# Performance work log

Measured on AMD Instinct MI355X. Metric: run time of the kernel, lower is better.

The kernel has to match this reference:

```python
import jax, jax.numpy as jnp
import numpy as np

B, N, D_IN, H = 4, 4096, 3072, 64
ADJ_DENSITY = 0.01


def _layernorm(x, g, b, eps=1e-5):
    mu = jnp.mean(x, axis=-1, keepdims=True)
    var = jnp.var(x, axis=-1, keepdims=True)
    return (x - mu) * jax.lax.rsqrt(var + eps) * g + b


def _gat(x, W, adj, concat):
    # x: [B, N, H], W: [H, H], adj: [N, N]
    Wh = jnp.matmul(x, W)                                   # [B, N, H]
    scores = jnp.einsum('bnh,bmh->bnm', Wh, Wh) / np.sqrt(H)  # [B, N, N]
    scores = jnp.where(adj > 0, scores, jnp.float32(-1e9))
    attn = jax.nn.softmax(scores, axis=2)                   # dropout: eval no-op
    h_prime = jnp.matmul(attn, Wh)                          # [B, N, H]
    return jax.nn.elu(h_prime) if concat else h_prime


def setup_inputs() -> dict:
    key = jax.random.key(0)
    ks = jax.random.split(key, 18)
    adj = (jax.random.uniform(ks[0], (N, N)) < ADJ_DENSITY).astype(jnp.float32)
    adj = jnp.maximum(adj, jnp.eye(N, dtype=jnp.float32))   # self loops

    def xavier(k, shape, gain=1.0):
        bound = gain * np.sqrt(6.0 / (shape[0] + shape[1]))
        return jax.random.uniform(k, shape, jnp.float32, -bound, bound)

    return {
        'stim_features': jax.random.normal(ks[1], (B, D_IN), jnp.float32),
        'adj': adj,
        'W_enc1': xavier(ks[2], (D_IN, 2 * H)),
        'b_enc1': jnp.zeros((2 * H,), jnp.float32),
        'ln_g': jnp.ones((2 * H,), jnp.float32),
        'ln_b': jnp.zeros((2 * H,), jnp.float32),
        'W_enc2': xavier(ks[3], (2 * H, H)),
        'b_enc2': jnp.zeros((H,), jnp.float32),
        'voxel_emb': jax.random.normal(ks[4], (N, H), jnp.float32) * 0.01,
        'W_gat1': xavier(ks[5], (H, H), gain=1.414),
        'W_gat2': xavier(ks[6], (H, H), gain=1.414),
        'skip1_W': xavier(ks[7], (H, H)),
        'skip1_b': jnp.zeros((H,), jnp.float32),
        'skip2_W': xavier(ks[8], (H, H)),
        'skip2_b': jnp.zeros((H,), jnp.float32),
        'ro_W': xavier(ks[9], (H, 1)),
        'ro_b': jnp.zeros((1,), jnp.float32),
    }


def reference(stim_features, adj, W_enc1, b_enc1, ln_g, ln_b, W_enc2, b_enc2,
              voxel_emb, W_gat1, W_gat2, skip1_W, skip1_b, skip2_W, skip2_b,
              ro_W, ro_b):
    # stim encoder: Linear -> LayerNorm -> GELU -> (Dropout eval) -> Linear
    g = stim_features @ W_enc1 + b_enc1                     # [B, 2H]
    g = _layernorm(g, ln_g, ln_b)
    g = jax.nn.gelu(g, approximate=False)
    g = g @ W_enc2 + b_enc2                                 # [B, H]

    x = g[:, None, :] + voxel_emb[None, :, :]               # [B, N, H]

    x_res = x
    x = _gat(x, W_gat1, adj, concat=True)
    x = x + (x_res @ skip1_W + skip1_b)

    x_res = x
    x = _gat(x, W_gat2, adj, concat=False)
    x = x + (x_res @ skip2_W + skip2_b)

    pred = (x @ ro_W + ro_b)[..., 0]                        # [B, N]
    return pred
```

## Files before the change

kernel.cpp:

```cpp
#include <hip/hip_runtime.h>
#include <math.h>

#define NB 4
#define NV 4096
#define DIN 3072
#define HD 64
#define CAP 80

typedef unsigned short u16;
typedef unsigned int u32;
typedef _Float16 h2 __attribute__((ext_vector_type(2)));

__device__ __forceinline__ float fdot2u(u32 v, u32 q, float c) {
#if __has_builtin(__builtin_amdgcn_fdot2)
  return __builtin_amdgcn_fdot2(__builtin_bit_cast(h2, v), __builtin_bit_cast(h2, q), c, false);
#else
  h2 a = __builtin_bit_cast(h2, v), b = __builtin_bit_cast(h2, q);
  return c + (float)a[0] * (float)b[0] + (float)a[1] * (float)b[1];
#endif
}

__device__ __forceinline__ h2 shx(h2 v, int off) {
  return __builtin_bit_cast(h2, (u32)__shfl_xor((int)__builtin_bit_cast(u32, v), off, 64));
}

__global__ __launch_bounds__(256) void pre_kernel(
    const float* __restrict__ adj, int* __restrict__ cnt, int* __restrict__ cols,
    const float* __restrict__ stim, const float* __restrict__ W1, float* __restrict__ part) {
  int bid = blockIdx.x;
  int t = threadIdx.x;
  if (bid < NV) {
    int row = bid;
    int l = t & 63, w = t >> 6;
    __shared__ int wtot[4];
    __shared__ int stot;
    const float4* p = (const float4*)(adj + (size_t)row * NV);
    float4 v0 = p[t], v1 = p[t + 256], v2 = p[t + 512], v3 = p[t + 768];
    int c = (v0.x > 0.f) + (v0.y > 0.f) + (v0.z > 0.f) + (v0.w > 0.f) +
            (v1.x > 0.f) + (v1.y > 0.f) + (v1.z > 0.f) + (v1.w > 0.f) +
            (v2.x > 0.f) + (v2.y > 0.f) + (v2.z > 0.f) + (v2.w > 0.f) +
            (v3.x > 0.f) + (v3.y > 0.f) + (v3.z > 0.f) + (v3.w > 0.f);
    int val = c;
#pragma unroll
    for (int off = 1; off < 64; off <<= 1) {
      int tmp = __shfl_up(val, off, 64);
      if (l >= off) val += tmp;
    }
    if (l == 63) wtot[w] = val;
    __syncthreads();
    int base = 0;
    for (int i = 0; i < w; ++i) base += wtot[i];
    if (t == 255) {
      int s = base + val;
      s = s > CAP ? CAP : s;
      cnt[row] = s;
      stot = s;
    }
    int o = base + (val - c);
    int* cr = cols + row * CAP;
#define EMIT(vv, jj) if ((vv) > 0.f) { if (o < CAP) cr[o] = (jj); ++o; }
    int j0 = t * 4, j1 = (t + 256) * 4, j2 = (t + 512) * 4, j3 = (t + 768) * 4;
    EMIT(v0.x, j0) EMIT(v0.y, j0 + 1) EMIT(v0.z, j0 + 2) EMIT(v0.w, j0 + 3)
    EMIT(v1.x, j1) EMIT(v1.y, j1 + 1) EMIT(v1.z, j1 + 2) EMIT(v1.w, j1 + 3)
    EMIT(v2.x, j2) EMIT(v2.y, j2 + 1) EMIT(v2.z, j2 + 2) EMIT(v2.w, j2 + 3)
    EMIT(v3.x, j3) EMIT(v3.y, j3 + 1) EMIT(v3.z, j3 + 2) EMIT(v3.w, j3 + 3)
#undef EMIT
    __syncthreads();
    if (t < CAP && t >= stot) cr[t] = 0;
  } else {
    int e = bid - NV;
    int c = e % 24;
    int b = e / 24;
    int j = t & 127, h = t >> 7;
    int k0 = c * 128 + h * 64;
    float acc = 0.f;
#pragma unroll 8
    for (int k = 0; k < 64; ++k)
      acc += stim[b * DIN + k0 + k] * W1[(size_t)(k0 + k) * 128 + j];
    part[((b * 24 + c) * 2 + h) * 128 + j] = acc;
  }
}

__global__ __launch_bounds__(128) void enc_b_kernel(
    const float* __restrict__ part, const float* __restrict__ b1,
    const float* __restrict__ lng, const float* __restrict__ lnb,
    const float* __restrict__ W2, const float* __restrict__ b2, float* __restrict__ g) {
  int b = blockIdx.x;
  int t = threadIdx.x;
  float hv = 0.f;
  for (int c = 0; c < 48; ++c) hv += part[(b * 48 + c) * 128 + t];
  hv += b1[t];
  __shared__ float act[128];
  __shared__ float red[128];
  __shared__ float s_mu, s_var;
  act[t] = hv;
  red[t] = hv;
  __syncthreads();
  for (int s = 64; s > 0; s >>= 1) {
    if (t < s) red[t] += red[t + s];
    __syncthreads();
  }
  if (t == 0) s_mu = red[0] * (1.f / 128.f);
  __syncthreads();
  float dv = act[t] - s_mu;
  red[t] = dv * dv;
  __syncthreads();
  for (int s = 64; s > 0; s >>= 1) {
    if (t < s) red[t] += red[t + s];
    __syncthreads();
  }
  if (t == 0) s_var = red[0] * (1.f / 128.f);
  __syncthreads();
  float y = (act[t] - s_mu) * rsqrtf(s_var + 1e-5f) * lng[t] + lnb[t];
  act[t] = 0.5f * y * (1.f + erff(y * 0.70710678118f));
  __syncthreads();
  if (t < 64) {
    float a2 = 0.f;
    for (int k = 0; k < 128; ++k) a2 += act[k] * W2[k * 64 + t];
    g[b * 64 + t] = a2 + b2[t];
  }
}

template <int LAYER>
__global__ __launch_bounds__(256) void whsk_kernel(
    const float* __restrict__ g, const float* __restrict__ emb, const float* __restrict__ xin,
    const float* __restrict__ Wg, const float* __restrict__ Sw, const float* __restrict__ Sb,
    u16* __restrict__ Whh, float* __restrict__ Sk) {
  __shared__ float wgt[4096];
  __shared__ float swt[4096];
  __shared__ float xst[64 * 33];
  __shared__ float sbs[64];
  int tid = threadIdx.x;
  for (int i = tid; i < 1024; i += 256) {
    ((float4*)wgt)[i] = ((const float4*)Wg)[i];
    ((float4*)swt)[i] = ((const float4*)Sw)[i];
  }
  if (tid < 64) sbs[tid] = Sb[tid];
  int base = blockIdx.x * 32;
  int b = base >> 12;
  for (int i4 = tid; i4 < 512; i4 += 256) {
    int rr = i4 >> 4, k0 = (i4 & 15) * 4;
    int grow = base + rr;
    float4 v;
    if (LAYER == 1) {
      int n = grow & (NV - 1);
      float4 gv = *(const float4*)(g + b * 64 + k0);
      float4 ev = *(const float4*)(emb + (size_t)n * 64 + k0);
      v = make_float4(gv.x + ev.x, gv.y + ev.y, gv.z + ev.z, gv.w + ev.w);
    } else {
      v = *(const float4*)(xin + (size_t)grow * 64 + k0);
    }
    xst[(k0 + 0) * 33 + rr] = v.x;
    xst[(k0 + 1) * 33 + rr] = v.y;
    xst[(k0 + 2) * 33 + rr] = v.z;
    xst[(k0 + 3) * 33 + rr] = v.w;
  }
  __syncthreads();
  int cg = tid & 15;
  int r0 = tid >> 4;
  float4 aw0 = make_float4(0, 0, 0, 0), as0 = make_float4(0, 0, 0, 0);
  float4 aw1 = make_float4(0, 0, 0, 0), as1 = make_float4(0, 0, 0, 0);
#pragma unroll 4
  for (int k = 0; k < 64; ++k) {
    float4 wv = *(const float4*)&wgt[k * 64 + 4 * cg];
    float4 sv = *(const float4*)&swt[k * 64 + 4 * cg];
    float x0 = xst[k * 33 + r0];
    float x1 = xst[k * 33 + r0 + 16];
    aw0.x = fmaf(x0, wv.x, aw0.x); aw0.y = fmaf(x0, wv.y, aw0.y);
    aw0.z = fmaf(x0, wv.z, aw0.z); aw0.w = fmaf(x0, wv.w, aw0.w);
    as0.x = fmaf(x0, sv.x, as0.x); as0.y = fmaf(x0, sv.y, as0.y);
    as0.z = fmaf(x0, sv.z, as0.z); as0.w = fmaf(x0, sv.w, as0.w);
    aw1.x = fmaf(x1, wv.x, aw1.x); aw1.y = fmaf(x1, wv.y, aw1.y);
    aw1.z = fmaf(x1, wv.z, aw1.z); aw1.w = fmaf(x1, wv.w, aw1.w);
    as1.x = fmaf(x1, sv.x, as1.x); as1.y = fmaf(x1, sv.y, as1.y);
    as1.z = fmaf(x1, sv.z, as1.z); as1.w = fmaf(x1, sv.w, as1.w);
  }
  float4 sb4 = *(const float4*)&sbs[4 * cg];
  int grow0 = base + r0, grow1 = base + r0 + 16;
  ushort4 h0, h1;
  h0.x = __builtin_bit_cast(u16, (_Float16)aw0.x);
  h0.y = __builtin_bit_cast(u16, (_Float16)aw0.y);
  h0.z = __builtin_bit_cast(u16, (_Float16)aw0.z);
  h0.w = __builtin_bit_cast(u16, (_Float16)aw0.w);
  h1.x = __builtin_bit_cast(u16, (_Float16)aw1.x);
  h1.y = __builtin_bit_cast(u16, (_Float16)aw1.y);
  h1.z = __builtin_bit_cast(u16, (_Float16)aw1.z);
  h1.w = __builtin_bit_cast(u16, (_Float16)aw1.w);
  *(ushort4*)(Whh + (size_t)grow0 * 64 + 4 * cg) = h0;
  *(ushort4*)(Whh + (size_t)grow1 * 64 + 4 * cg) = h1;
  *(float4*)(Sk + (size_t)grow0 * 64 + 4 * cg) =
      make_float4(as0.x + sb4.x, as0.y + sb4.y, as0.z + sb4.z, as0.w + sb4.w);
  *(float4*)(Sk + (size_t)grow1 * 64 + 4 * cg) =
      make_float4(as1.x + sb4.x, as1.y + sb4.y, as1.z + sb4.z, as1.w + sb4.w);
}

template <bool ELU1>
__global__ __launch_bounds__(256) void attn_kernel(
    const u16* __restrict__ Whh, const float* __restrict__ Sk,
    const int* __restrict__ cnt, const int* __restrict__ cols, float* __restrict__ xout,
    const float* __restrict__ roW, const float* __restrict__ rob, float* __restrict__ out) {
  int tid = threadIdx.x;
  int lane = tid & 63;
  int w = tid >> 6;
  int bid = blockIdx.x;
  int x = bid & 7;
  int gidx = bid >> 3;
  int b = x >> 1;
  int n = __builtin_amdgcn_readfirstlane((x & 1) * 2048 + gidx * 4 + w);
  int wid = b * NV + n;
  const u16* whhbase = Whh + (size_t)b * (NV * HD);
  int nn = __builtin_amdgcn_readfirstlane(cnt[n]);
  const int* cl = cols + n * CAP;
  int q = lane & 3;
  int gq = lane >> 2;

  const uint4* qr = (const uint4*)(whhbase + (size_t)n * HD);
  uint4 QA = qr[q];
  uint4 QB = qr[q + 4];

  float s[5], p[5];
  uint4 SA0, SB0, SA1, SB1, SA2, SB2;
#define SCORE_BLOCK(jb, SAv, SBv)                                                                \
  {                                                                                              \
    int j = (jb) * 16 + gq;                                                                      \
    int m = cl[j];                                                                               \
    const uint4* vr = (const uint4*)(whhbase + (size_t)m * HD);                                  \
    SAv = vr[q];                                                                                 \
    SBv = vr[q + 4];                                                                             \
    float t = 0.f;                                                                               \
    t = fdot2u(SAv.x, QA.x, t);                                                                  \
    t = fdot2u(SAv.y, QA.y, t);                                                                  \
    t = fdot2u(SAv.z, QA.z, t);                                                                  \
    t = fdot2u(SAv.w, QA.w, t);                                                                  \
    t = fdot2u(SBv.x, QB.x, t);                                                                  \
    t = fdot2u(SBv.y, QB.y, t);                                                                  \
    t = fdot2u(SBv.z, QB.z, t);                                                                  \
    t = fdot2u(SBv.w, QB.w, t);                                                                  \
    t += __shfl_xor(t, 1, 64);                                                                   \
    t += __shfl_xor(t, 2, 64);                                                                   \
    s[jb] = (j < nn) ? t * 0.125f : -1e30f;                                                      \
  }

  SCORE_BLOCK(0, SA0, SB0)
  SCORE_BLOCK(1, SA1, SB1)
  SCORE_BLOCK(2, SA2, SB2)
  s[3] = -1e30f;
  s[4] = -1e30f;
  bool tail = (nn > 48);
  if (tail) {
    uint4 TA, TB;
    SCORE_BLOCK(3, TA, TB)
    SCORE_BLOCK(4, TA, TB)
  }
#undef SCORE_BLOCK

  float mx = fmaxf(fmaxf(fmaxf(s[0], s[1]), fmaxf(s[2], s[3])), s[4]);
  mx = fmaxf(mx, __shfl_xor(mx, 4, 64));
  mx = fmaxf(mx, __shfl_xor(mx, 8, 64));
  mx = fmaxf(mx, __shfl_xor(mx, 16, 64));
  mx = fmaxf(mx, __shfl_xor(mx, 32, 64));
  float sum = 0.f;
#pragma unroll
  for (int jb = 0; jb < 5; ++jb) {
    p[jb] = (jb * 16 + gq < nn) ? __expf(s[jb] - mx) : 0.f;
    sum += p[jb];
  }
  sum += __shfl_xor(sum, 4, 64);
  sum += __shfl_xor(sum, 8, 64);
  sum += __shfl_xor(sum, 16, 64);
  sum += __shfl_xor(sum, 32, 64);
  float inv = 1.f / sum;

  h2 aa[8];
#pragma unroll
  for (int k = 0; k < 8; ++k) aa[k] = h2{(_Float16)0, (_Float16)0};
#define PV_ACC(pp, Av, Bv)                                                                       \
  {                                                                                              \
    _Float16 pf = (_Float16)(pp);                                                                \
    h2 ph = {pf, pf};                                                                            \
    aa[0] += __builtin_bit_cast(h2, (Av).x) * ph;                                                \
    aa[1] += __builtin_bit_cast(h2, (Av).y) * ph;                                                \
    aa[2] += __builtin_bit_cast(h2, (Av).z) * ph;                                                \
    aa[3] += __builtin_bit_cast(h2, (Av).w) * ph;                                                \
    aa[4] += __builtin_bit_cast(h2, (Bv).x) * ph;                                                \
    aa[5] += __builtin_bit_cast(h2, (Bv).y) * ph;                                                \
    aa[6] += __builtin_bit_cast(h2, (Bv).z) * ph;                                                \
    aa[7] += __builtin_bit_cast(h2, (Bv).w) * ph;                                                \
  }
  PV_ACC(p[0], SA0, SB0)
  PV_ACC(p[1], SA1, SB1)
  PV_ACC(p[2], SA2, SB2)
  if (tail) {
    int m3 = cl[48 + gq];
    const uint4* vr3 = (const uint4*)(whhbase + (size_t)m3 * HD);
    uint4 A3 = vr3[q], B3 = vr3[q + 4];
    PV_ACC(p[3], A3, B3)
    if (nn > 64) {
      int m4 = cl[64 + gq];
      const uint4* vr4 = (const uint4*)(whhbase + (size_t)m4 * HD);
      uint4 A4 = vr4[q], B4 = vr4[q + 4];
      PV_ACC(p[4], A4, B4)
    }
  }
#undef PV_ACC

  bool g1 = (gq & 1) != 0;
  h2 bb[4];
#pragma unroll
  for (int i = 0; i < 4; ++i) {
    h2 k = g1 ? aa[i + 4] : aa[i];
    h2 u = g1 ? aa[i] : aa[i + 4];
    bb[i] = k + shx(u, 4);
  }
  bool g2 = (gq & 2) != 0;
  h2 cc[2];
#pragma unroll
  for (int i = 0; i < 2; ++i) {
    h2 k = g2 ? bb[i + 2] : bb[i];
    h2 u = g2 ? bb[i] : bb[i + 2];
    cc[i] = k + shx(u, 8);
  }
  bool g4 = (gq & 4) != 0;
  h2 dd;
  {
    h2 k = g4 ? cc[1] : cc[0];
    h2 u = g4 ? cc[0] : cc[1];
    dd = k + shx(u, 16);
  }
  dd = dd + shx(dd, 32);
  int a = 8 * q + 32 * (gq & 1) + 4 * ((gq >> 1) & 1) + 2 * ((gq >> 2) & 1);
  float f0 = (float)dd[0] * inv;
  float f1 = (float)dd[1] * inv;

  size_t obase = (size_t)wid * HD;
  float2 sk2 = *(const float2*)(Sk + obase + a);
  if (ELU1) {
    float o0 = (f0 > 0.f ? f0 : (__expf(f0) - 1.f)) + sk2.x;
    float o1 = (f1 > 0.f ? f1 : (__expf(f1) - 1.f)) + sk2.y;
    if ((gq & 8) == 0) *(float2*)(xout + obase + a) = make_float2(o0, o1);
  } else {
    float2 ro2 = *(const float2*)(roW + a);
    float wsp = (f0 + sk2.x) * ro2.x + (f1 + sk2.y) * ro2.y;
    wsp += __shfl_xor(wsp, 1, 64);
    wsp += __shfl_xor(wsp, 2, 64);
    wsp += __shfl_xor(wsp, 4, 64);
    wsp += __shfl_xor(wsp, 8, 64);
    wsp += __shfl_xor(wsp, 16, 64);
    if (lane == 0) out[wid] = wsp + rob[0];
  }
}

extern "C" void kernel_launch(void* const* d_in, const int* in_sizes, int n_in,
                              void* d_out, int out_size, void* d_ws, size_t ws_size,
                              hipStream_t stream) {
  const float* stim = (const float*)d_in[0];
  const float* adj  = (const float*)d_in[1];
  const float* W1   = (const float*)d_in[2];
  const float* b1   = (const float*)d_in[3];
  const float* lng  = (const float*)d_in[4];
  const float* lnb  = (const float*)d_in[5];
  const float* W2   = (const float*)d_in[6];
  const float* b2   = (const float*)d_in[7];
  const float* emb  = (const float*)d_in[8];
  const float* Wg1  = (const float*)d_in[9];
  const float* Wg2  = (const float*)d_in[10];
  const float* s1w  = (const float*)d_in[11];
  const float* s1b  = (const float*)d_in[12];
  const float* s2w  = (const float*)d_in[13];
  const float* s2b  = (const float*)d_in[14];
  const float* roW  = (const float*)d_in[15];
  const float* rob  = (const float*)d_in[16];
  float* out = (float*)d_out;

  char* ws = (char*)d_ws;
  float* g    = (float*)(ws + 0);
  float* part = (float*)(ws + 4096);
  int*   cnt  = (int*)(ws + 131072);
  int*   cols = (int*)(ws + 147456);
  float* Sk   = (float*)(ws + 5767168);
  float* x1   = (float*)(ws + 9961472);
  u16*   Whh  = (u16*)(ws + 14155776);

  pre_kernel<<<dim3(NV + 96), dim3(256), 0, stream>>>(adj, cnt, cols, stim, W1, part);
  enc_b_kernel<<<dim3(4), dim3(128), 0, stream>>>(part, b1, lng, lnb, W2, b2, g);
  whsk_kernel<1><<<dim3(NB * NV / 32), dim3(256), 0, stream>>>(g, emb, (const float*)nullptr,
                                                               Wg1, s1w, s1b, Whh, Sk);
  attn_kernel<true><<<dim3(NB * NV / 4), dim3(256), 0, stream>>>(Whh, Sk, cnt, cols, x1,
                                                                 roW, rob, (float*)nullptr);
  whsk_kernel<2><<<dim3(NB * NV / 32), dim3(256), 0, stream>>>(g, emb, x1, Wg2, s2w, s2b,
                                                               Whh, Sk);
  attn_kernel<false><<<dim3(NB * NV / 4), dim3(256), 0, stream>>>(Whh, Sk, cnt, cols,
                                                                  (float*)nullptr, roW, rob, out);
}
```

Measured before the change: 62.78 us.

## Fuse encoder tail into layer-1 projection and layer-2 projection into layer-1 attention

```diff
diff --git a/kernel.cpp b/kernel.cpp
--- a/kernel.cpp
+++ b/kernel.cpp
@@ -81,79 +81,72 @@
   }
 }
 
-__global__ __launch_bounds__(128) void enc_b_kernel(
+__global__ __launch_bounds__(256) void whsk1_kernel(
     const float* __restrict__ part, const float* __restrict__ b1,
     const float* __restrict__ lng, const float* __restrict__ lnb,
-    const float* __restrict__ W2, const float* __restrict__ b2, float* __restrict__ g) {
-  int b = blockIdx.x;
-  int t = threadIdx.x;
-  float hv = 0.f;
-  for (int c = 0; c < 48; ++c) hv += part[(b * 48 + c) * 128 + t];
-  hv += b1[t];
-  __shared__ float act[128];
-  __shared__ float red[128];
-  __shared__ float s_mu, s_var;
-  act[t] = hv;
-  red[t] = hv;
-  __syncthreads();
-  for (int s = 64; s > 0; s >>= 1) {
-    if (t < s) red[t] += red[t + s];
-    __syncthreads();
-  }
-  if (t == 0) s_mu = red[0] * (1.f / 128.f);
-  __syncthreads();
-  float dv = act[t] - s_mu;
-  red[t] = dv * dv;
-  __syncthreads();
-  for (int s = 64; s > 0; s >>= 1) {
-    if (t < s) red[t] += red[t + s];
-    __syncthreads();
-  }
-  if (t == 0) s_var = red[0] * (1.f / 128.f);
-  __syncthreads();
-  float y = (act[t] - s_mu) * rsqrtf(s_var + 1e-5f) * lng[t] + lnb[t];
-  act[t] = 0.5f * y * (1.f + erff(y * 0.70710678118f));
-  __syncthreads();
-  if (t < 64) {
-    float a2 = 0.f;
-    for (int k = 0; k < 128; ++k) a2 += act[k] * W2[k * 64 + t];
-    g[b * 64 + t] = a2 + b2[t];
-  }
-}
-
-template <int LAYER>
-__global__ __launch_bounds__(256) void whsk_kernel(
-    const float* __restrict__ g, const float* __restrict__ emb, const float* __restrict__ xin,
-    const float* __restrict__ Wg, const float* __restrict__ Sw, const float* __restrict__ Sb,
+    const float* __restrict__ W2, const float* __restrict__ b2,
+    const float* __restrict__ emb, const float* __restrict__ Wg,
+    const float* __restrict__ Sw, const float* __restrict__ Sb,
     u16* __restrict__ Whh, float* __restrict__ Sk) {
   __shared__ float wgt[4096];
   __shared__ float swt[4096];
   __shared__ float xst[64 * 33];
   __shared__ float sbs[64];
+  __shared__ float act[128];
+  __shared__ float red[128];
+  __shared__ __align__(16) float gs[64];
+  __shared__ float s_mu, s_var;
   int tid = threadIdx.x;
+  int base = blockIdx.x * 32;
+  int b = base >> 12;
+
   for (int i = tid; i < 1024; i += 256) {
     ((float4*)wgt)[i] = ((const float4*)Wg)[i];
     ((float4*)swt)[i] = ((const float4*)Sw)[i];
   }
   if (tid < 64) sbs[tid] = Sb[tid];
-  int base = blockIdx.x * 32;
-  int b = base >> 12;
+  if (tid < 128) {
+    float hv = 0.f;
+    for (int c = 0; c < 48; ++c) hv += part[(b * 48 + c) * 128 + tid];
+    hv += b1[tid];
+    act[tid] = hv;
+    red[tid] = hv;
+  }
+  __syncthreads();
+  for (int s = 64; s > 0; s >>= 1) {
+    if (tid < s) red[tid] += red[tid + s];
+    __syncthreads();
+  }
+  if (tid == 0) s_mu = red[0] * (1.f / 128.f);
+  __syncthreads();
+  if (tid < 128) { float dv = act[tid] - s_mu; red[tid] = dv * dv; }
+  __syncthreads();
+  for (int s = 64; s > 0; s >>= 1) {
+    if (tid < s) red[tid] += red[tid + s];
+    __syncthreads();
+  }
+  if (tid == 0) s_var = red[0] * (1.f / 128.f);
+  __syncthreads();
+  if (tid < 128) {
+    float y = (act[tid] - s_mu) * rsqrtf(s_var + 1e-5f) * lng[tid] + lnb[tid];
+    act[tid] = 0.5f * y * (1.f + erff(y * 0.70710678118f));
+  }
+  __syncthreads();
+  if (tid < 64) {
+    float a2 = 0.f;
+    for (int k = 0; k < 128; ++k) a2 += act[k] * W2[k * 64 + tid];
+    gs[tid] = a2 + b2[tid];
+  }
+  __syncthreads();
   for (int i4 = tid; i4 < 512; i4 += 256) {
     int rr = i4 >> 4, k0 = (i4 & 15) * 4;
-    int grow = base + rr;
-    float4 v;
-    if (LAYER == 1) {
-      int n = grow & (NV - 1);
-      float4 gv = *(const float4*)(g + b * 64 + k0);
-      float4 ev = *(const float4*)(emb + (size_t)n * 64 + k0);
-      v = make_float4(gv.x + ev.x, gv.y + ev.y, gv.z + ev.z, gv.w + ev.w);
-    } else {
-      v = *(const float4*)(xin + (size_t)grow * 64 + k0);
-    }
-    xst[(k0 + 0) * 33 + rr] = v.x;
-    xst[(k0 + 1) * 33 + rr] = v.y;
-    xst[(k0 + 2) * 33 + rr] = v.z;
-    xst[(k0 + 3) * 33 + rr] = v.w;
+    int n = (base + rr) & (NV - 1);
+    float4 gv = *(const float4*)(gs + k0);
+    float4 ev = *(const float4*)(emb + (size_t)n * 64 + k0);
+    xst[(k0 + 0) * 33 + rr] = gv.x + ev.x;
+    xst[(k0 + 1) * 33 + rr] = gv.y + ev.y;
+    xst[(k0 + 2) * 33 + rr] = gv.z + ev.z;
+    xst[(k0 + 3) * 33 + rr] = gv.w + ev.w;
   }
   __syncthreads();
   int cg = tid & 15;
@@ -165,15 +158,15 @@
     float4 wv = *(const float4*)&wgt[k * 64 + 4 * cg];
     float4 sv = *(const float4*)&swt[k * 64 + 4 * cg];
     float x0 = xst[k * 33 + r0];
-    float x1 = xst[k * 33 + r0 + 16];
+    float x1v = xst[k * 33 + r0 + 16];
     aw0.x = fmaf(x0, wv.x, aw0.x); aw0.y = fmaf(x0, wv.y, aw0.y);
     aw0.z = fmaf(x0, wv.z, aw0.z); aw0.w = fmaf(x0, wv.w, aw0.w);
     as0.x = fmaf(x0, sv.x, as0.x); as0.y = fmaf(x0, sv.y, as0.y);
     as0.z = fmaf(x0, sv.z, as0.z); as0.w = fmaf(x0, sv.w, as0.w);
-    aw1.x = fmaf(x1, wv.x, aw1.x); aw1.y = fmaf(x1, wv.y, aw1.y);
-    aw1.z = fmaf(x1, wv.z, aw1.z); aw1.w = fmaf(x1, wv.w, aw1.w);
-    as1.x = fmaf(x1, sv.x, as1.x); as1.y = fmaf(x1, sv.y, as1.y);
-    as1.z = fmaf(x1, sv.z, as1.z); as1.w = fmaf(x1, sv.w, as1.w);
+    aw1.x = fmaf(x1v, wv.x, aw1.x); aw1.y = fmaf(x1v, wv.y, aw1.y);
+    aw1.z = fmaf(x1v, wv.z, aw1.z); aw1.w = fmaf(x1v, wv.w, aw1.w);
+    as1.x = fmaf(x1v, sv.x, as1.x); as1.y = fmaf(x1v, sv.y, as1.y);
+    as1.z = fmaf(x1v, sv.z, as1.z); as1.w = fmaf(x1v, sv.w, as1.w);
   }
   float4 sb4 = *(const float4*)&sbs[4 * cg];
   int grow0 = base + r0, grow1 = base + r0 + 16;
@@ -194,11 +187,15 @@
       make_float4(as1.x + sb4.x, as1.y + sb4.y, as1.z + sb4.z, as1.w + sb4.w);
 }
 
-template <bool ELU1>
-__global__ __launch_bounds__(256) void attn_kernel(
+__global__ __launch_bounds__(512) void attn_l1_kernel(
     const u16* __restrict__ Whh, const float* __restrict__ Sk,
-    const int* __restrict__ cnt, const int* __restrict__ cols, float* __restrict__ xout,
-    const float* __restrict__ roW, const float* __restrict__ rob, float* __restrict__ out) {
+    const int* __restrict__ cnt, const int* __restrict__ cols,
+    const float* __restrict__ Wg2, const float* __restrict__ Sw2, const float* __restrict__ Sb2,
+    u16* __restrict__ Whh2, float* __restrict__ Sk2) {
+  __shared__ float wgt[4096];
+  __shared__ float swt[4096];
+  __shared__ float sbs[64];
+  __shared__ float xl[8][64];
   int tid = threadIdx.x;
   int lane = tid & 63;
   int w = tid >> 6;
@@ -206,13 +203,20 @@
   int x = bid & 7;
   int gidx = bid >> 3;
   int b = x >> 1;
-  int n = __builtin_amdgcn_readfirstlane((x & 1) * 2048 + gidx * 4 + w);
+  int rowhalf = x & 1;
+  int n = __builtin_amdgcn_readfirstlane(rowhalf * 2048 + gidx * 8 + w);
   int wid = b * NV + n;
   const u16* whhbase = Whh + (size_t)b * (NV * HD);
   int nn = __builtin_amdgcn_readfirstlane(cnt[n]);
   const int* cl = cols + n * CAP;
   int q = lane & 3;
   int gq = lane >> 2;
+
+  for (int i = tid; i < 1024; i += 512) {
+    ((float4*)wgt)[i] = ((const float4*)Wg2)[i];
+    ((float4*)swt)[i] = ((const float4*)Sw2)[i];
+  }
+  if (tid < 64) sbs[tid] = Sb2[tid];
 
   const uint4* qr = (const uint4*)(whhbase + (size_t)n * HD);
   uint4 QA = qr[q];
@@ -240,7 +244,6 @@
     t += __shfl_xor(t, 2, 64);                                                                   \
     s[jb] = (j < nn) ? t * 0.125f : -1e30f;                                                      \
   }
-
   SCORE_BLOCK(0, SA0, SB0)
   SCORE_BLOCK(1, SA1, SB1)
   SCORE_BLOCK(2, SA2, SB2)
@@ -332,22 +335,188 @@
   float f0 = (float)dd[0] * inv;
   float f1 = (float)dd[1] * inv;
 
-  size_t obase = (size_t)wid * HD;
-  float2 sk2 = *(const float2*)(Sk + obase + a);
-  if (ELU1) {
-    float o0 = (f0 > 0.f ? f0 : (__expf(f0) - 1.f)) + sk2.x;
-    float o1 = (f1 > 0.f ? f1 : (__expf(f1) - 1.f)) + sk2.y;
-    if ((gq & 8) == 0) *(float2*)(xout + obase + a) = make_float2(o0, o1);
-  } else {
-    float2 ro2 = *(const float2*)(roW + a);
-    float wsp = (f0 + sk2.x) * ro2.x + (f1 + sk2.y) * ro2.y;
-    wsp += __shfl_xor(wsp, 1, 64);
-    wsp += __shfl_xor(wsp, 2, 64);
-    wsp += __shfl_xor(wsp, 4, 64);
-    wsp += __shfl_xor(wsp, 8, 64);
-    wsp += __shfl_xor(wsp, 16, 64);
-    if (lane == 0) out[wid] = wsp + rob[0];
-  }
+  float2 sk2 = *(const float2*)(Sk + (size_t)wid * HD + a);
+  float o0 = (f0 > 0.f ? f0 : (__expf(f0) - 1.f)) + sk2.x;
+  float o1 = (f1 > 0.f ? f1 : (__expf(f1) - 1.f)) + sk2.y;
+  if ((gq & 8) == 0) {
+    xl[w][a] = o0;
+    xl[w][a + 1] = o1;
+  }
+  __syncthreads();
+
+  if (tid < 128) {
+    int cg = tid & 15;
+    int r = tid >> 4;
+    float4 aw = make_float4(0, 0, 0, 0), as = make_float4(0, 0, 0, 0);
+#pragma unroll 4
+    for (int k = 0; k < 64; ++k) {
+      float4 wv = *(const float4*)&wgt[k * 64 + 4 * cg];
+      float4 sv = *(const float4*)&swt[k * 64 + 4 * cg];
+      float xv = xl[r][k];
+      aw.x = fmaf(xv, wv.x, aw.x); aw.y = fmaf(xv, wv.y, aw.y);
+      aw.z = fmaf(xv, wv.z, aw.z); aw.w = fmaf(xv, wv.w, aw.w);
+      as.x = fmaf(xv, sv.x, as.x); as.y = fmaf(xv, sv.y, as.y);
+      as.z = fmaf(xv, sv.z, as.z); as.w = fmaf(xv, sv.w, as.w);
+    }
+    int n_r = rowhalf * 2048 + gidx * 8 + r;
+    size_t wid_r = (size_t)(b * NV + n_r) * 64 + 4 * cg;
+    float4 sb4 = *(const float4*)&sbs[4 * cg];
+    ushort4 hh;
+    hh.x = __builtin_bit_cast(u16, (_Float16)aw.x);
+    hh.y = __builtin_bit_cast(u16, (_Float16)aw.y);
+    hh.z = __builtin_bit_cast(u16, (_Float16)aw.z);
+    hh.w = __builtin_bit_cast(u16, (_Float16)aw.w);
+    *(ushort4*)(Whh2 + wid_r) = hh;
+    *(float4*)(Sk2 + wid_r) =
+        make_float4(as.x + sb4.x, as.y + sb4.y, as.z + sb4.z, as.w + sb4.w);
+  }
+}
+
+__global__ __launch_bounds__(256) void attn_l2_kernel(
+    const u16* __restrict__ Whh, const float* __restrict__ Sk,
+    const int* __restrict__ cnt, const int* __restrict__ cols,
+    const float* __restrict__ roW, const float* __restrict__ rob, float* __restrict__ out) {
+  int tid = threadIdx.x;
+  int lane = tid & 63;
+  int w = tid >> 6;
+  int bid = blockIdx.x;
+  int x = bid & 7;
+  int gidx = bid >> 3;
+  int b = x >> 1;
+  int n = __builtin_amdgcn_readfirstlane((x & 1) * 2048 + gidx * 4 + w);
+  int wid = b * NV + n;
+  const u16* whhbase = Whh + (size_t)b * (NV * HD);
+  int nn = __builtin_amdgcn_readfirstlane(cnt[n]);
+  const int* cl = cols + n * CAP;
+  int q = lane & 3;
+  int gq = lane >> 2;
+
+  const uint4* qr = (const uint4*)(whhbase + (size_t)n * HD);
+  uint4 QA = qr[q];
+  uint4 QB = qr[q + 4];
+
+  float s[5], p[5];
+  uint4 SA0, SB0, SA1, SB1, SA2, SB2;
+#define SCORE_BLOCK(jb, SAv, SBv)                                                                \
+  {                                                                                              \
+    int j = (jb) * 16 + gq;                                                                      \
+    int m = cl[j];                                                                               \
+    const uint4* vr = (const uint4*)(whhbase + (size_t)m * HD);                                  \
+    SAv = vr[q];                                                                                 \
+    SBv = vr[q + 4];                                                                             \
+    float t = 0.f;                                                                               \
+    t = fdot2u(SAv.x, QA.x, t);                                                                  \
+    t = fdot2u(SAv.y, QA.y, t);                                                                  \
+    t = fdot2u(SAv.z, QA.z, t);                                                                  \
+    t = fdot2u(SAv.w, QA.w, t);                                                                  \
+    t = fdot2u(SBv.x, QB.x, t);                                                                  \
+    t = fdot2u(SBv.y, QB.y, t);                                                                  \
+    t = fdot2u(SBv.z, QB.z, t);                                                                  \
+    t = fdot2u(SBv.w, QB.w, t);                                                                  \
+    t += __shfl_xor(t, 1, 64);                                                                   \
+    t += __shfl_xor(t, 2, 64);                                                                   \
+    s[jb] = (j < nn) ? t * 0.125f : -1e30f;                                                      \
+  }
+  SCORE_BLOCK(0, SA0, SB0)
+  SCORE_BLOCK(1, SA1, SB1)
+  SCORE_BLOCK(2, SA2, SB2)
+  s[3] = -1e30f;
+  s[4] = -1e30f;
+  bool tail = (nn > 48);
+  if (tail) {
+    uint4 TA, TB;
+    SCORE_BLOCK(3, TA, TB)
+    SCORE_BLOCK(4, TA, TB)
+  }
+#undef SCORE_BLOCK
+
+  float mx = fmaxf(fmaxf(fmaxf(s[0], s[1]), fmaxf(s[2], s[3])), s[4]);
+  mx = fmaxf(mx, __shfl_xor(mx, 4, 64));
+  mx = fmaxf(mx, __shfl_xor(mx, 8, 64));
+  mx = fmaxf(mx, __shfl_xor(mx, 16, 64));
+  mx = fmaxf(mx, __shfl_xor(mx, 32, 64));
+  float sum = 0.f;
+#pragma unroll
+  for (int jb = 0; jb < 5; ++jb) {
+    p[jb] = (jb * 16 + gq < nn) ? __expf(s[jb] - mx) : 0.f;
+    sum += p[jb];
+  }
+  sum += __shfl_xor(sum, 4, 64);
+  sum += __shfl_xor(sum, 8, 64);
+  sum += __shfl_xor(sum, 16, 64);
+  sum += __shfl_xor(sum, 32, 64);
+  float inv = 1.f / sum;
+
+  h2 aa[8];
+#pragma unroll
+  for (int k = 0; k < 8; ++k) aa[k] = h2{(_Float16)0, (_Float16)0};
+#define PV_ACC(pp, Av, Bv)                                                                       \
+  {                                                                                              \
+    _Float16 pf = (_Float16)(pp);                                                                \
+    h2 ph = {pf, pf};                                                                            \
+    aa[0] += __builtin_bit_cast(h2, (Av).x) * ph;                                                \
+    aa[1] += __builtin_bit_cast(h2, (Av).y) * ph;                                                \
+    aa[2] += __builtin_bit_cast(h2, (Av).z) * ph;                                                \
+    aa[3] += __builtin_bit_cast(h2, (Av).w) * ph;                                                \
+    aa[4] += __builtin_bit_cast(h2, (Bv).x) * ph;                                                \
+    aa[5] += __builtin_bit_cast(h2, (Bv).y) * ph;                                                \
+    aa[6] += __builtin_bit_cast(h2, (Bv).z) * ph;                                                \
+    aa[7] += __builtin_bit_cast(h2, (Bv).w) * ph;                                                \
+  }
+  PV_ACC(p[0], SA0, SB0)
+  PV_ACC(p[1], SA1, SB1)
+  PV_ACC(p[2], SA2, SB2)
+  if (tail) {
+    int m3 = cl[48 + gq];
+    const uint4* vr3 = (const uint4*)(whhbase + (size_t)m3 * HD);
+    uint4 A3 = vr3[q], B3 = vr3[q + 4];
+    PV_ACC(p[3], A3, B3)
+    if (nn > 64) {
+      int m4 = cl[64 + gq];
+      const uint4* vr4 = (const uint4*)(whhbase + (size_t)m4 * HD);
+      uint4 A4 = vr4[q], B4 = vr4[q + 4];
+      PV_ACC(p[4], A4, B4)
+    }
+  }
+#undef PV_ACC
+
+  bool g1 = (gq & 1) != 0;
+  h2 bb[4];
+#pragma unroll
+  for (int i = 0; i < 4; ++i) {
+    h2 k = g1 ? aa[i + 4] : aa[i];
+    h2 u = g1 ? aa[i] : aa[i + 4];
+    bb[i] = k + shx(u, 4);
+  }
+  bool g2 = (gq & 2) != 0;
+  h2 cc[2];
+#pragma unroll
+  for (int i = 0; i < 2; ++i) {
+    h2 k = g2 ? bb[i + 2] : bb[i];
+    h2 u = g2 ? bb[i] : bb[i + 2];
+    cc[i] = k + shx(u, 8);
+  }
+  bool g4 = (gq & 4) != 0;
+  h2 dd;
+  {
+    h2 k = g4 ? cc[1] : cc[0];
+    h2 u = g4 ? cc[0] : cc[1];
+    dd = k + shx(u, 16);
+  }
+  dd = dd + shx(dd, 32);
+  int a = 8 * q + 32 * (gq & 1) + 4 * ((gq >> 1) & 1) + 2 * ((gq >> 2) & 1);
+  float f0 = (float)dd[0] * inv;
+  float f1 = (float)dd[1] * inv;
+
+  float2 sk2 = *(const float2*)(Sk + (size_t)wid * HD + a);
+  float2 ro2 = *(const float2*)(roW + a);
+  float wsp = (f0 + sk2.x) * ro2.x + (f1 + sk2.y) * ro2.y;
+  wsp += __shfl_xor(wsp, 1, 64);
+  wsp += __shfl_xor(wsp, 2, 64);
+  wsp += __shfl_xor(wsp, 4, 64);
+  wsp += __shfl_xor(wsp, 8, 64);
+  wsp += __shfl_xor(wsp, 16, 64);
+  if (lane == 0) out[wid] = wsp + rob[0];
 }
 
 extern "C" void kernel_launch(void* const* d_in, const int* in_sizes, int n_in,
@@ -373,22 +542,19 @@
   float* out = (float*)d_out;
 
   char* ws = (char*)d_ws;
-  float* g    = (float*)(ws + 0);
   float* part = (float*)(ws + 4096);
   int*   cnt  = (int*)(ws + 131072);
   int*   cols = (int*)(ws + 147456);
+  u16*   Whh2 = (u16*)(ws + 1572864);
   float* Sk   = (float*)(ws + 5767168);
-  float* x1   = (float*)(ws + 9961472);
+  float* Sk2  = (float*)(ws + 9961472);
   u16*   Whh  = (u16*)(ws + 14155776);
 
   pre_kernel<<<dim3(NV + 96), dim3(256), 0, stream>>>(adj, cnt, cols, stim, W1, part);
-  enc_b_kernel<<<dim3(4), dim3(128), 0, stream>>>(part, b1, lng, lnb, W2, b2, g);
-  whsk_kernel<1><<<dim3(NB * NV / 32), dim3(256), 0, stream>>>(g, emb, (const float*)nullptr,
-                                                               Wg1, s1w, s1b, Whh, Sk);
-  attn_kernel<true><<<dim3(NB * NV / 4), dim3(256), 0, stream>>>(Whh, Sk, cnt, cols, x1,
-                                                                 roW, rob, (float*)nullptr);
-  whsk_kernel<2><<<dim3(NB * NV / 32), dim3(256), 0, stream>>>(g, emb, x1, Wg2, s2w, s2b,
-                                                               Whh, Sk);
-  attn_kernel<false><<<dim3(NB * NV / 4), dim3(256), 0, stream>>>(Whh, Sk, cnt, cols,
-                                                                  (float*)nullptr, roW, rob, out);
-}
+  whsk1_kernel<<<dim3(NB * NV / 32), dim3(256), 0, stream>>>(part, b1, lng, lnb, W2, b2,
+                                                             emb, Wg1, s1w, s1b, Whh, Sk);
+  attn_l1_kernel<<<dim3(NB * NV / 8), dim3(512), 0, stream>>>(Whh, Sk, cnt, cols,
+                                                              Wg2, s2w, s2b, Whh2, Sk2);
+  attn_l2_kernel<<<dim3(NB * NV / 4), dim3(256), 0, stream>>>(Whh2, Sk2, cnt, cols,
+                                                              roW, rob, out);
+}
```

Result: faster. 61.13 us (-2.6%).
